# Kernel tuning notes

Measured on AMD Instinct MI355X. Metric: run time of the kernel, lower is better.

The kernel has to match this reference:

```python
import jax, jax.numpy as jnp
import numpy as np

T, B = 1024, 32
Q1, K1, V1 = 1024, 1024, 1024
Q2, K2, V2 = 1024, 1024, 1024
KW = 3  # kernel_width
EPS = 1e-6


def mask_softmax(x, mask):
    # softmax over dim 0 with multiplicative mask (exp(x-max)*mask / sum)
    e = jnp.exp(x - jnp.max(x, axis=0, keepdims=True))
    e = e * mask
    return e / jnp.sum(e, axis=0, keepdims=True)


def setup_inputs() -> dict:
    key = jax.random.key(0)
    ks = jax.random.split(key, 16)
    s = 0.02
    return {
        "q1": jax.random.normal(ks[0], (B, Q1), jnp.float32),
        "k1": jax.random.normal(ks[1], (T, B, K1), jnp.float32),
        "v1": jax.random.normal(ks[2], (T, B, V1), jnp.float32),
        "q2": jax.random.normal(ks[3], (B, Q2), jnp.float32),
        "k2": jax.random.normal(ks[4], (T, B, K2), jnp.float32),
        "v2": jax.random.normal(ks[5], (T, B, V2), jnp.float32),
        "k_mask": jnp.ones((T, B), jnp.float32),
        # Attention params: sa: Linear(q1_size -> align_size=K1); a1: Linear(K1 -> 1)
        "sa_w": jax.random.normal(ks[6], (K1, Q1), jnp.float32) * s,
        "sa_b": jnp.zeros((K1,), jnp.float32),
        "a1_w": jax.random.normal(ks[7], (1, K1), jnp.float32) * s,
        "a1_b": jnp.zeros((1,), jnp.float32),
        # AttCNN4Weight: q_to_kernel: Linear(q2_size -> k2_size*KW)
        "qk_w": jax.random.normal(ks[8], (K2 * KW, Q2), jnp.float32) * s,
        "qk_b": jnp.zeros((K2 * KW,), jnp.float32),
        # LayerNorm(v1_size)
        "ln_g": jnp.ones((V1,), jnp.float32),
        "ln_b": jnp.zeros((V1,), jnp.float32),
    }


def reference(q1, k1, v1, q2, k2, v2, k_mask,
              sa_w, sa_b, a1_w, a1_b, qk_w, qk_b, ln_g, ln_b):
    # ---- additive attention path ----
    # tanh(sa(q1)[None] + k1): [T, B, K1]
    t = jnp.tanh((q1 @ sa_w.T + sa_b)[None, :, :] + k1)
    a_1 = jnp.einsum('tba,a->tb', t, a1_w[0]) + a1_b[0]          # [T, B]
    e_1 = mask_softmax(a_1, k_mask)
    attend_1 = jnp.einsum('tb,tbd->bd', e_1, v1)                  # [B, V1]

    # ---- dynamic grouped-conv1d attention path ----
    kernel = (q2 @ qk_w.T + qk_b).reshape(B, K2, KW)              # per-example kernels
    pad = (KW - 1) // 2
    k2p = jnp.pad(k2, ((pad, pad), (0, 0), (0, 0)))               # [T+2p, B, K2]
    a_2 = jnp.zeros((T, B), k2.dtype)
    for w in range(KW):  # tiny fixed loop over kernel taps
        a_2 = a_2 + jnp.einsum('tbc,bc->tb', k2p[w:w + T], kernel[:, :, w])
    e_2 = mask_softmax(a_2, k_mask)
    attend_2 = jnp.einsum('tb,tbd->bd', e_2, v2)                  # [B, V2]

    # ---- combine: add + LayerNorm over feature dim ----
    x = attend_1 + attend_2
    mu = jnp.mean(x, axis=-1, keepdims=True)
    var = jnp.mean((x - mu) ** 2, axis=-1, keepdims=True)
    combined = (x - mu) * jax.lax.rsqrt(var + EPS) * ln_g + ln_b
    return combined
```

## Files before the change

kernel.cpp:

```cpp
#include <hip/hip_runtime.h>
#include <math.h>

#define T_DIM   1024
#define B_DIM   32
#define N_FEAT  1024
#define KW      3
#define NT      32
#define T_PER   (T_DIM / NT)
#define EPS     1e-6f

__device__ __forceinline__ float tanh_fast(float x) {
  float ax = fminf(fabsf(x), 10.f);
  float e  = __expf(ax + ax);
  float r  = fmaf(-2.f, __builtin_amdgcn_rcpf(e + 1.f), 1.f);
  return copysignf(r, x);
}

__global__ void __launch_bounds__(256) prep_kernel(
    const float* __restrict__ q1, const float* __restrict__ sa_w,
    const float* __restrict__ sa_b, const float* __restrict__ q2,
    const float* __restrict__ qk_w, const float* __restrict__ qk_b,
    float* __restrict__ sa_q, float* __restrict__ kern_t) {
  int wid  = (blockIdx.x * 256 + threadIdx.x) >> 6;
  int lane = threadIdx.x & 63;
  int b = wid & (B_DIM - 1);
  int m = wid >> 5;
  const float4* xr;
  const float4* wr;
  if (m < 1024) {
    xr = (const float4*)(q1 + (size_t)b * N_FEAT);
    wr = (const float4*)(sa_w + (size_t)m * N_FEAT);
  } else {
    xr = (const float4*)(q2 + (size_t)b * N_FEAT);
    wr = (const float4*)(qk_w + (size_t)(m - 1024) * N_FEAT);
  }
  float acc = 0.f;
#pragma unroll
  for (int i = 0; i < 4; i++) {
    float4 xv = xr[lane + 64 * i], wv = wr[lane + 64 * i];
    acc += xv.x * wv.x + xv.y * wv.y + xv.z * wv.z + xv.w * wv.w;
  }
#pragma unroll
  for (int off = 32; off > 0; off >>= 1) acc += __shfl_down(acc, off, 64);
  if (lane == 0) {
    if (m < 1024) {
      sa_q[(size_t)b * N_FEAT + m] = acc + sa_b[m];
    } else {
      int mm = m - 1024;
      int c = mm / 3, w = mm - 3 * c;
      kern_t[(size_t)b * (N_FEAT * KW) + (size_t)w * N_FEAT + c] = acc + qk_b[mm];
    }
  }
}

__global__ void __launch_bounds__(256) row_dots_kernel(
    const float* __restrict__ k1, const float* __restrict__ k2,
    const float* __restrict__ sa_q, const float* __restrict__ a1_w,
    const float* __restrict__ kern_t, const float* __restrict__ a1_b,
    float* __restrict__ a1_out, float* __restrict__ s_out) {
  int blk = blockIdx.x;
  int b   = blk & (B_DIM - 1);
  int tid = threadIdx.x;
  size_t row = (size_t)blk * N_FEAT + tid * 4;
  int f = tid * 4;

  float4 k1v = *(const float4*)(k1 + row);
  float4 sqv = *(const float4*)(sa_q + (size_t)b * N_FEAT + f);
  float4 awv = *(const float4*)(a1_w + f);
  float p1 = tanh_fast(k1v.x + sqv.x) * awv.x
           + tanh_fast(k1v.y + sqv.y) * awv.y
           + tanh_fast(k1v.z + sqv.z) * awv.z
           + tanh_fast(k1v.w + sqv.w) * awv.w;

  float4 k2v = *(const float4*)(k2 + row);
  const float* kb = kern_t + (size_t)b * (N_FEAT * KW);
  float4 w0 = *(const float4*)(kb + 0 * N_FEAT + f);
  float4 w1 = *(const float4*)(kb + 1 * N_FEAT + f);
  float4 w2 = *(const float4*)(kb + 2 * N_FEAT + f);
  float s0 = k2v.x * w0.x + k2v.y * w0.y + k2v.z * w0.z + k2v.w * w0.w;
  float s1 = k2v.x * w1.x + k2v.y * w1.y + k2v.z * w1.z + k2v.w * w1.w;
  float s2 = k2v.x * w2.x + k2v.y * w2.y + k2v.z * w2.z + k2v.w * w2.w;

  float vals[4] = {p1, s0, s1, s2};
#pragma unroll
  for (int off = 32; off > 0; off >>= 1) {
#pragma unroll
    for (int j = 0; j < 4; j++) vals[j] += __shfl_down(vals[j], off, 64);
  }
  __shared__ float red[4][4];
  int wave = tid >> 6, lane = tid & 63;
  if (lane == 0) {
#pragma unroll
    for (int j = 0; j < 4; j++) red[wave][j] = vals[j];
  }
  __syncthreads();
  if (tid == 0) {
    float r0 = red[0][0] + red[1][0] + red[2][0] + red[3][0];
    float r1 = red[0][1] + red[1][1] + red[2][1] + red[3][1];
    float r2 = red[0][2] + red[1][2] + red[2][2] + red[3][2];
    float r3 = red[0][3] + red[1][3] + red[2][3] + red[3][3];
    a1_out[blk] = r0 + a1_b[0];
    s_out[(size_t)blk * 3 + 0] = r1;
    s_out[(size_t)blk * 3 + 1] = r2;
    s_out[(size_t)blk * 3 + 2] = r3;
  }
}

__device__ __forceinline__ float block_reduce_256(float v, bool is_max,
                                                  float* sm ) {
#pragma unroll
  for (int off = 32; off > 0; off >>= 1) {
    float o = __shfl_down(v, off, 64);
    v = is_max ? fmaxf(v, o) : v + o;
  }
  int wave = threadIdx.x >> 6;
  if ((threadIdx.x & 63) == 0) sm[wave] = v;
  __syncthreads();
  float r = is_max ? fmaxf(fmaxf(sm[0], sm[1]), fmaxf(sm[2], sm[3]))
                   : sm[0] + sm[1] + sm[2] + sm[3];
  __syncthreads();
  return r;
}

__global__ void __launch_bounds__(256) softmax_kernel(
    const float* __restrict__ a1, const float* __restrict__ s,
    const float* __restrict__ k_mask,
    float* __restrict__ e1, float* __restrict__ e2) {
  int b = blockIdx.x;
  int tid = threadIdx.x;
  __shared__ float sm[4];

  float x1[4], x2[4], mk[4];
#pragma unroll
  for (int k = 0; k < 4; k++) {
    int t = tid + k * 256;
    x1[k] = a1[(size_t)t * B_DIM + b];
    float sl = (t > 0)         ? s[((size_t)(t - 1) * B_DIM + b) * 3 + 0] : 0.f;
    float sc =                   s[((size_t)t       * B_DIM + b) * 3 + 1];
    float sr = (t < T_DIM - 1) ? s[((size_t)(t + 1) * B_DIM + b) * 3 + 2] : 0.f;
    x2[k] = sl + sc + sr;
    mk[k] = k_mask[(size_t)t * B_DIM + b];
  }
  float m1 = fmaxf(fmaxf(x1[0], x1[1]), fmaxf(x1[2], x1[3]));
  float m2 = fmaxf(fmaxf(x2[0], x2[1]), fmaxf(x2[2], x2[3]));
  m1 = block_reduce_256(m1, true, sm);
  m2 = block_reduce_256(m2, true, sm);

  float v1[4], v2[4], sum1 = 0.f, sum2 = 0.f;
#pragma unroll
  for (int k = 0; k < 4; k++) {
    v1[k] = __expf(x1[k] - m1) * mk[k];
    v2[k] = __expf(x2[k] - m2) * mk[k];
    sum1 += v1[k];
    sum2 += v2[k];
  }
  sum1 = block_reduce_256(sum1, false, sm);
  sum2 = block_reduce_256(sum2, false, sm);
  float i1 = 1.f / sum1, i2 = 1.f / sum2;
#pragma unroll
  for (int k = 0; k < 4; k++) {
    int t = tid + k * 256;
    e1[(size_t)t * B_DIM + b] = v1[k] * i1;
    e2[(size_t)t * B_DIM + b] = v2[k] * i2;
  }
}

__global__ void __launch_bounds__(256) weighted_v_kernel(
    const float* __restrict__ v1, const float* __restrict__ v2,
    const float* __restrict__ e1, const float* __restrict__ e2,
    float* __restrict__ partial) {
  int b  = blockIdx.x;
  int tc = blockIdx.y;
  int tid = threadIdx.x;
  __shared__ float se1[T_PER], se2[T_PER];
  if (tid < T_PER)
    se1[tid] = e1[(size_t)(tc * T_PER + tid) * B_DIM + b];
  else if (tid < 2 * T_PER)
    se2[tid - T_PER] = e2[(size_t)(tc * T_PER + (tid - T_PER)) * B_DIM + b];
  __syncthreads();

  float4 acc1 = {0.f, 0.f, 0.f, 0.f}, acc2 = {0.f, 0.f, 0.f, 0.f};
  size_t dofs = (size_t)tid * 4;
#pragma unroll 8
  for (int i = 0; i < T_PER; i++) {
    size_t row = ((size_t)(tc * T_PER + i) * B_DIM + b) * N_FEAT + dofs;
    float4 a = *(const float4*)(v1 + row);
    float4 c = *(const float4*)(v2 + row);
    float w1 = se1[i], w2 = se2[i];
    acc1.x = fmaf(w1, a.x, acc1.x); acc1.y = fmaf(w1, a.y, acc1.y);
    acc1.z = fmaf(w1, a.z, acc1.z); acc1.w = fmaf(w1, a.w, acc1.w);
    acc2.x = fmaf(w2, c.x, acc2.x); acc2.y = fmaf(w2, c.y, acc2.y);
    acc2.z = fmaf(w2, c.z, acc2.z); acc2.w = fmaf(w2, c.w, acc2.w);
  }
  size_t o1 = ((size_t)(0 * NT + tc) * B_DIM + b) * N_FEAT + dofs;
  size_t o2 = ((size_t)(1 * NT + tc) * B_DIM + b) * N_FEAT + dofs;
  *(float4*)(partial + o1) = acc1;
  *(float4*)(partial + o2) = acc2;
}

__device__ __forceinline__ float block_reduce_sum_1024(float v, float* sm) {
#pragma unroll
  for (int off = 32; off > 0; off >>= 1) v += __shfl_down(v, off, 64);
  int wave = threadIdx.x >> 6;
  if ((threadIdx.x & 63) == 0) sm[wave] = v;
  __syncthreads();
  float tot = 0.f;
#pragma unroll
  for (int i = 0; i < 16; i++) tot += sm[i];
  __syncthreads();
  return tot;
}

__global__ void __launch_bounds__(1024) ln_kernel(
    const float* __restrict__ partial, const float* __restrict__ ln_g,
    const float* __restrict__ ln_b, float* __restrict__ out) {
  int b = blockIdx.x;
  int d = threadIdx.x;
  __shared__ float sm[16];
  float x = 0.f;
#pragma unroll
  for (int j = 0; j < 2 * NT; j++)
    x += partial[((size_t)j * B_DIM + b) * N_FEAT + d];
  float ssum = block_reduce_sum_1024(x, sm);
  float mu = ssum * (1.f / N_FEAT);
  float dx = x - mu;
  float vsum = block_reduce_sum_1024(dx * dx, sm);
  float inv = rsqrtf(vsum * (1.f / N_FEAT) + EPS);
  out[(size_t)b * N_FEAT + d] = dx * inv * ln_g[d] + ln_b[d];
}

extern "C" void kernel_launch(void* const* d_in, const int* in_sizes, int n_in,
                              void* d_out, int out_size, void* d_ws, size_t ws_size,
                              hipStream_t stream) {
  const float* q1     = (const float*)d_in[0];
  const float* k1     = (const float*)d_in[1];
  const float* v1     = (const float*)d_in[2];
  const float* q2     = (const float*)d_in[3];
  const float* k2     = (const float*)d_in[4];
  const float* v2     = (const float*)d_in[5];
  const float* k_mask = (const float*)d_in[6];
  const float* sa_w   = (const float*)d_in[7];
  const float* sa_b   = (const float*)d_in[8];
  const float* a1_w   = (const float*)d_in[9];
  const float* a1_b   = (const float*)d_in[10];
  const float* qk_w   = (const float*)d_in[11];
  const float* qk_b   = (const float*)d_in[12];
  const float* ln_g   = (const float*)d_in[13];
  const float* ln_bp  = (const float*)d_in[14];
  float* out = (float*)d_out;
  float* ws  = (float*)d_ws;

  float* sa_q    = ws;
  float* kern_t  = sa_q + 32768;
  float* s       = kern_t + 98304;
  float* a1      = s + 98304;
  float* e1      = a1 + 32768;
  float* e2      = e1 + 32768;
  float* partial = e2 + 32768;

  prep_kernel<<<dim3((4096 * B_DIM) / 4), 256, 0, stream>>>(
      q1, sa_w, sa_b, q2, qk_w, qk_b, sa_q, kern_t);
  row_dots_kernel<<<dim3(T_DIM * B_DIM), 256, 0, stream>>>(
      k1, k2, sa_q, a1_w, kern_t, a1_b, a1, s);
  softmax_kernel<<<dim3(B_DIM), 256, 0, stream>>>(a1, s, k_mask, e1, e2);
  weighted_v_kernel<<<dim3(B_DIM, NT), 256, 0, stream>>>(v1, v2, e1, e2, partial);
  ln_kernel<<<dim3(B_DIM), 1024, 0, stream>>>(partial, ln_g, ln_bp, out);
}
```

Baseline: 538.1 us.

## Make row-dot kernel persistent with prefetch and interleave weighted-V rows

The row-dots kernel now launches 2048 persistent blocks that each loop over 16 strided rows. Per-batch weights are loaded once per block, and the next k1/k2 row is prefetched while the current one is reduced, with a double-buffered shared reduction array. The weighted-V kernel now has each block walk rows strided across the whole T range, so concurrently running blocks read contiguous memory, and it register-prefetches the next row. The aim is lower launch and scheduling overhead plus better memory-level parallelism on this bandwidth-bound work, at the cost of a __syncthreads per row and fewer blocks in flight.

Result: no change. 537.4 us (-0.1%).

```diff
diff --git a/kernel.cpp b/kernel.cpp
--- a/kernel.cpp
+++ b/kernel.cpp
@@ -6,8 +6,12 @@
 #define N_FEAT  1024
 #define KW      3
 #define NT      32
-#define T_PER   (T_DIM / NT)
 #define EPS     1e-6f
+
+#define RD_BLOCKS 2048
+#define RD_RPB    (T_DIM * B_DIM / RD_BLOCKS)
+#define WV_BLOCKS (B_DIM * NT)
+#define WV_RPB    (T_DIM / NT)
 
 __device__ __forceinline__ float tanh_fast(float x) {
   float ax = fminf(fabsf(x), 10.f);
@@ -53,56 +57,66 @@
   }
 }
 
-__global__ void __launch_bounds__(256) row_dots_kernel(
+__global__ void __launch_bounds__(256, 4) row_dots_kernel(
     const float* __restrict__ k1, const float* __restrict__ k2,
     const float* __restrict__ sa_q, const float* __restrict__ a1_w,
     const float* __restrict__ kern_t, const float* __restrict__ a1_b,
     float* __restrict__ a1_out, float* __restrict__ s_out) {
-  int blk = blockIdx.x;
-  int b   = blk & (B_DIM - 1);
+  int g   = blockIdx.x;
+  int b   = g & (B_DIM - 1);
   int tid = threadIdx.x;
-  size_t row = (size_t)blk * N_FEAT + tid * 4;
-  int f = tid * 4;
-
-  float4 k1v = *(const float4*)(k1 + row);
+  int f   = tid * 4;
+  int wave = tid >> 6, lane = tid & 63;
+  __shared__ float red[2][4][4];
+
   float4 sqv = *(const float4*)(sa_q + (size_t)b * N_FEAT + f);
   float4 awv = *(const float4*)(a1_w + f);
-  float p1 = tanh_fast(k1v.x + sqv.x) * awv.x
-           + tanh_fast(k1v.y + sqv.y) * awv.y
-           + tanh_fast(k1v.z + sqv.z) * awv.z
-           + tanh_fast(k1v.w + sqv.w) * awv.w;
-
-  float4 k2v = *(const float4*)(k2 + row);
   const float* kb = kern_t + (size_t)b * (N_FEAT * KW);
   float4 w0 = *(const float4*)(kb + 0 * N_FEAT + f);
   float4 w1 = *(const float4*)(kb + 1 * N_FEAT + f);
   float4 w2 = *(const float4*)(kb + 2 * N_FEAT + f);
-  float s0 = k2v.x * w0.x + k2v.y * w0.y + k2v.z * w0.z + k2v.w * w0.w;
-  float s1 = k2v.x * w1.x + k2v.y * w1.y + k2v.z * w1.z + k2v.w * w1.w;
-  float s2 = k2v.x * w2.x + k2v.y * w2.y + k2v.z * w2.z + k2v.w * w2.w;
-
-  float vals[4] = {p1, s0, s1, s2};
-#pragma unroll
-  for (int off = 32; off > 0; off >>= 1) {
-#pragma unroll
-    for (int j = 0; j < 4; j++) vals[j] += __shfl_down(vals[j], off, 64);
-  }
-  __shared__ float red[4][4];
-  int wave = tid >> 6, lane = tid & 63;
-  if (lane == 0) {
-#pragma unroll
-    for (int j = 0; j < 4; j++) red[wave][j] = vals[j];
-  }
-  __syncthreads();
-  if (tid == 0) {
-    float r0 = red[0][0] + red[1][0] + red[2][0] + red[3][0];
-    float r1 = red[0][1] + red[1][1] + red[2][1] + red[3][1];
-    float r2 = red[0][2] + red[1][2] + red[2][2] + red[3][2];
-    float r3 = red[0][3] + red[1][3] + red[2][3] + red[3][3];
-    a1_out[blk] = r0 + a1_b[0];
-    s_out[(size_t)blk * 3 + 0] = r1;
-    s_out[(size_t)blk * 3 + 1] = r2;
-    s_out[(size_t)blk * 3 + 2] = r3;
+  float a1bv = a1_b[0];
+
+  float4 c1 = *(const float4*)(k1 + (size_t)g * N_FEAT + f);
+  float4 c2 = *(const float4*)(k2 + (size_t)g * N_FEAT + f);
+
+  for (int i = 0; i < RD_RPB; i++) {
+    int r  = g + (i << 11);
+    int rn = (i + 1 < RD_RPB) ? r + RD_BLOCKS : r;
+    float4 n1 = *(const float4*)(k1 + (size_t)rn * N_FEAT + f);
+    float4 n2 = *(const float4*)(k2 + (size_t)rn * N_FEAT + f);
+
+    float p1 = tanh_fast(c1.x + sqv.x) * awv.x
+             + tanh_fast(c1.y + sqv.y) * awv.y
+             + tanh_fast(c1.z + sqv.z) * awv.z
+             + tanh_fast(c1.w + sqv.w) * awv.w;
+    float s0 = c2.x * w0.x + c2.y * w0.y + c2.z * w0.z + c2.w * w0.w;
+    float s1 = c2.x * w1.x + c2.y * w1.y + c2.z * w1.z + c2.w * w1.w;
+    float s2 = c2.x * w2.x + c2.y * w2.y + c2.z * w2.z + c2.w * w2.w;
+
+    float vals[4] = {p1, s0, s1, s2};
+#pragma unroll
+    for (int off = 32; off > 0; off >>= 1) {
+#pragma unroll
+      for (int j = 0; j < 4; j++) vals[j] += __shfl_down(vals[j], off, 64);
+    }
+    int ph = i & 1;
+    if (lane == 0) {
+#pragma unroll
+      for (int j = 0; j < 4; j++) red[ph][wave][j] = vals[j];
+    }
+    __syncthreads();
+    if (tid == 0) {
+      float r0 = red[ph][0][0] + red[ph][1][0] + red[ph][2][0] + red[ph][3][0];
+      float r1 = red[ph][0][1] + red[ph][1][1] + red[ph][2][1] + red[ph][3][1];
+      float r2 = red[ph][0][2] + red[ph][1][2] + red[ph][2][2] + red[ph][3][2];
+      float r3 = red[ph][0][3] + red[ph][1][3] + red[ph][2][3] + red[ph][3][3];
+      a1_out[r] = r0 + a1bv;
+      s_out[(size_t)r * 3 + 0] = r1;
+      s_out[(size_t)r * 3 + 1] = r2;
+      s_out[(size_t)r * 3 + 2] = r3;
+    }
+    c1 = n1; c2 = n2;
   }
 }
 
@@ -169,31 +183,35 @@
     const float* __restrict__ v1, const float* __restrict__ v2,
     const float* __restrict__ e1, const float* __restrict__ e2,
     float* __restrict__ partial) {
-  int b  = blockIdx.x;
-  int tc = blockIdx.y;
-  int tid = threadIdx.x;
-  __shared__ float se1[T_PER], se2[T_PER];
-  if (tid < T_PER)
-    se1[tid] = e1[(size_t)(tc * T_PER + tid) * B_DIM + b];
-  else if (tid < 2 * T_PER)
-    se2[tid - T_PER] = e2[(size_t)(tc * T_PER + (tid - T_PER)) * B_DIM + b];
-  __syncthreads();
-
+  int g     = blockIdx.x;
+  int b     = g & (B_DIM - 1);
+  int chunk = g >> 5;
+  int tid   = threadIdx.x;
+  size_t f  = (size_t)tid * 4;
+  __shared__ float se1[WV_RPB], se2[WV_RPB];
+  if (tid < WV_RPB)
+    se1[tid] = e1[(size_t)(chunk + tid * NT) * B_DIM + b];
+  else if (tid < 2 * WV_RPB)
+    se2[tid - WV_RPB] = e2[(size_t)(chunk + (tid - WV_RPB) * NT) * B_DIM + b];
+  __syncthreads();
+
+  float4 c1 = *(const float4*)(v1 + (size_t)g * N_FEAT + f);
+  float4 c2 = *(const float4*)(v2 + (size_t)g * N_FEAT + f);
   float4 acc1 = {0.f, 0.f, 0.f, 0.f}, acc2 = {0.f, 0.f, 0.f, 0.f};
-  size_t dofs = (size_t)tid * 4;
-#pragma unroll 8
-  for (int i = 0; i < T_PER; i++) {
-    size_t row = ((size_t)(tc * T_PER + i) * B_DIM + b) * N_FEAT + dofs;
-    float4 a = *(const float4*)(v1 + row);
-    float4 c = *(const float4*)(v2 + row);
+  for (int i = 0; i < WV_RPB; i++) {
+    int r  = g + (i << 10);
+    int rn = (i + 1 < WV_RPB) ? r + WV_BLOCKS : r;
+    float4 n1 = *(const float4*)(v1 + (size_t)rn * N_FEAT + f);
+    float4 n2 = *(const float4*)(v2 + (size_t)rn * N_FEAT + f);
     float w1 = se1[i], w2 = se2[i];
-    acc1.x = fmaf(w1, a.x, acc1.x); acc1.y = fmaf(w1, a.y, acc1.y);
-    acc1.z = fmaf(w1, a.z, acc1.z); acc1.w = fmaf(w1, a.w, acc1.w);
-    acc2.x = fmaf(w2, c.x, acc2.x); acc2.y = fmaf(w2, c.y, acc2.y);
-    acc2.z = fmaf(w2, c.z, acc2.z); acc2.w = fmaf(w2, c.w, acc2.w);
-  }
-  size_t o1 = ((size_t)(0 * NT + tc) * B_DIM + b) * N_FEAT + dofs;
-  size_t o2 = ((size_t)(1 * NT + tc) * B_DIM + b) * N_FEAT + dofs;
+    acc1.x = fmaf(w1, c1.x, acc1.x); acc1.y = fmaf(w1, c1.y, acc1.y);
+    acc1.z = fmaf(w1, c1.z, acc1.z); acc1.w = fmaf(w1, c1.w, acc1.w);
+    acc2.x = fmaf(w2, c2.x, acc2.x); acc2.y = fmaf(w2, c2.y, acc2.y);
+    acc2.z = fmaf(w2, c2.z, acc2.z); acc2.w = fmaf(w2, c2.w, acc2.w);
+    c1 = n1; c2 = n2;
+  }
+  size_t o1 = ((size_t)(0 * NT + chunk) * B_DIM + b) * N_FEAT + f;
+  size_t o2 = ((size_t)(1 * NT + chunk) * B_DIM + b) * N_FEAT + f;
   *(float4*)(partial + o1) = acc1;
   *(float4*)(partial + o2) = acc2;
 }
@@ -260,9 +278,9 @@
 
   prep_kernel<<<dim3((4096 * B_DIM) / 4), 256, 0, stream>>>(
       q1, sa_w, sa_b, q2, qk_w, qk_b, sa_q, kern_t);
-  row_dots_kernel<<<dim3(T_DIM * B_DIM), 256, 0, stream>>>(
+  row_dots_kernel<<<dim3(RD_BLOCKS), 256, 0, stream>>>(
       k1, k2, sa_q, a1_w, kern_t, a1_b, a1, s);
   softmax_kernel<<<dim3(B_DIM), 256, 0, stream>>>(a1, s, k_mask, e1, e2);
-  weighted_v_kernel<<<dim3(B_DIM, NT), 256, 0, stream>>>(v1, v2, e1, e2, partial);
+  weighted_v_kernel<<<dim3(WV_BLOCKS), 256, 0, stream>>>(v1, v2, e1, e2, partial);
   ln_kernel<<<dim3(B_DIM), 1024, 0, stream>>>(partial, ln_g, ln_bp, out);
 }
```
